# Performance work log

Measured on AMD Instinct MI355X. Metric: run time of the kernel, lower is better.

The kernel has to match this reference:

```python
import jax, jax.numpy as jnp
import numpy as np
import math
from jax import lax

B, NP1, M, D, H, L, DFF = 16, 65, 256, 512, 8, 3, 2048
EPS_PROJ = 0.01  # MartingaleProjectionLayer is built with epsilon=0.01
LN_EPS = 1e-5


def _pos_encoding(n, d):
    pos = np.arange(n, dtype=np.float32)[:, None]
    div = np.exp(np.arange(0, d, 2, dtype=np.float32) * (-math.log(10000.0) / d))
    pe = np.zeros((n, d), dtype=np.float32)
    pe[:, 0::2] = np.sin(pos * div)
    pe[:, 1::2] = np.cos(pos * div)
    return jnp.asarray(pe)


def setup_inputs() -> dict:
    key = jax.random.key(0)
    ks = jax.random.split(key, 32)
    s = 0.02
    marg = jax.random.uniform(ks[0], (B, NP1, M), jnp.float32)
    marg = marg / marg.sum(axis=-1, keepdims=True)  # proper distributions
    return {
        "marginals": marg,
        "x_grid": jnp.linspace(-3.0, 3.0, M, dtype=jnp.float32),
        "conv_w": jax.random.normal(ks[1], (128, 1, 5), jnp.float32) * s,
        "conv_b": jax.random.normal(ks[2], (128,), jnp.float32) * s,
        "fc_w": jax.random.normal(ks[3], (128, D), jnp.float32) * s,
        "fc_b": jax.random.normal(ks[4], (D,), jnp.float32) * s,
        "ln0_g": jnp.ones((D,), jnp.float32),
        "ln0_b": jnp.zeros((D,), jnp.float32),
        "pos_enc": _pos_encoding(NP1, D),
        "qkv_w": jax.random.normal(ks[5], (L, 3 * D, D), jnp.float32) * s,
        "qkv_b": jax.random.normal(ks[6], (L, 3 * D), jnp.float32) * s,
        "out_w": jax.random.normal(ks[7], (L, D, D), jnp.float32) * s,
        "out_b": jax.random.normal(ks[8], (L, D), jnp.float32) * s,
        "ln1_g": jnp.ones((L, D), jnp.float32),
        "ln1_b": jnp.zeros((L, D), jnp.float32),
        "ff1_w": jax.random.normal(ks[9], (L, DFF, D), jnp.float32) * s,
        "ff1_b": jax.random.normal(ks[10], (L, DFF), jnp.float32) * s,
        "ff2_w": jax.random.normal(ks[11], (L, D, DFF), jnp.float32) * s,
        "ff2_b": jax.random.normal(ks[12], (L, D), jnp.float32) * s,
        "ln2_g": jnp.ones((L, D), jnp.float32),
        "ln2_b": jnp.zeros((L, D), jnp.float32),
        "u_w": jax.random.normal(ks[13], (M, D), jnp.float32) * s,
        "u_b": jax.random.normal(ks[14], (M,), jnp.float32) * s,
        "h_w": jax.random.normal(ks[15], (M, D), jnp.float32) * s,
        "h_b": jax.random.normal(ks[16], (M,), jnp.float32) * s,
    }


def _ln(x, g, b):
    mu = x.mean(axis=-1, keepdims=True)
    var = ((x - mu) ** 2).mean(axis=-1, keepdims=True)
    return (x - mu) * lax.rsqrt(var + LN_EPS) * g + b


def _gelu(x):
    return jax.nn.gelu(x, approximate=False)  # torch default exact GELU


def reference(marginals, x_grid, conv_w, conv_b, fc_w, fc_b, ln0_g, ln0_b,
              pos_enc, qkv_w, qkv_b, out_w, out_b, ln1_g, ln1_b,
              ff1_w, ff1_b, ff2_w, ff2_b, ln2_g, ln2_b, u_w, u_b, h_w, h_b):
    b, np1, m = marginals.shape
    n = np1 - 1
    d = fc_w.shape[1]
    nh = H
    dh = d // nh

    # ---- marginal embedding: Conv1d(1,128,k=5,pad=2) -> mean over grid -> FC+LN+GELU
    x = marginals.reshape(b * np1, 1, m)
    y = lax.conv_general_dilated(x, conv_w, (1,), [(2, 2)],
                                 dimension_numbers=("NCH", "OIH", "NCH"))
    y = y + conv_b[None, :, None]          # (b*np1, 128, m)
    emb = y.mean(axis=2)                   # (b*np1, 128)
    emb = _gelu(_ln(emb @ fc_w + fc_b, ln0_g, ln0_b))
    xs = emb.reshape(b, np1, d) + pos_enc[None, :np1, :]

    # ---- post-norm transformer encoder (dropout off / eval mode)
    scale = 1.0 / math.sqrt(dh)
    for l in range(L):
        qkv = xs @ qkv_w[l].T + qkv_b[l]                        # (b, s, 3d)
        q, k, v = jnp.split(qkv, 3, axis=-1)
        q = q.reshape(b, np1, nh, dh).transpose(0, 2, 1, 3)
        k = k.reshape(b, np1, nh, dh).transpose(0, 2, 1, 3)
        v = v.reshape(b, np1, nh, dh).transpose(0, 2, 1, 3)
        att = jax.nn.softmax(jnp.einsum("bhqd,bhkd->bhqk", q, k) * scale, axis=-1)
        o = jnp.einsum("bhqk,bhkd->bhqd", att, v)
        o = o.transpose(0, 2, 1, 3).reshape(b, np1, d)
        o = o @ out_w[l].T + out_b[l]
        xs = _ln(xs + o, ln1_g[l], ln1_b[l])
        ff = _gelu(xs @ ff1_w[l].T + ff1_b[l]) @ ff2_w[l].T + ff2_b[l]
        xs = _ln(xs + ff, ln2_g[l], ln2_b[l])

    u_pot = xs @ u_w.T + u_b                                    # (b, np1, M)
    h_raw = xs[:, :n, :] @ h_w.T + h_b                          # (b, n, M)

    # ---- vectorized martingale projection over all N timesteps
    x_diff = x_grid[:, None] - x_grid[None, :]                  # (M, M)
    h_kernel = h_raw[..., None] * x_diff                        # (b, n, M, M)
    P = jax.nn.softmax(h_kernel / EPS_PROJ, axis=-1)
    expected_next = jnp.einsum("bnij,j->bni", P, x_grid)
    drift = expected_next - x_grid                              # (b, n, M)
    mu = marginals[:, :n, :]
    weight_drift = (mu * drift).sum(axis=-1, keepdims=True)
    correction = weight_drift / (mu.sum(axis=-1, keepdims=True) + 1e-8)
    h_pot = h_raw - correction
    return (u_pot, h_pot)
```

## Files before the change

### kernel.cpp

```cpp
#include <hip/hip_runtime.h>
#include <math.h>


#define BT   1040
#define NP1  65
#define Dm   512
#define MG   256

typedef short short8 __attribute__((ext_vector_type(8)));
typedef float f32x4  __attribute__((ext_vector_type(4)));
typedef unsigned short u16;

__device__ __forceinline__ size_t pidx(int r, int c, int KB) {
  return ((size_t)((r >> 6) * KB + (c >> 6)) * 8 + ((c & 63) >> 3)) * 512
       + (size_t)((r & 63) * 8 + (c & 7));
}

__device__ __forceinline__ u16 f2bf(float f) {
  unsigned int u = __float_as_uint(f);
  u += 0x7FFF + ((u >> 16) & 1);
  return (u16)(u >> 16);
}

__device__ __forceinline__ float bf2f(u16 v) {
  return __uint_as_float((unsigned int)v << 16);
}

__device__ __forceinline__ float gelu_exact(float x) {
  return 0.5f * x * (1.0f + erff(x * 0.70710678118654752f));
}

__device__ __forceinline__ void async16(const u16* g, u16* l) {
  __builtin_amdgcn_global_load_lds(
      (const __attribute__((address_space(1))) unsigned int*)g,
      (__attribute__((address_space(3))) unsigned int*)l, 16, 0, 0);
}

__device__ __forceinline__ float wred(float v) {
#pragma unroll
  for (int o = 32; o; o >>= 1) v += __shfl_xor(v, o, 64);
  return v;
}

__device__ __forceinline__ float block_reduce_sum(float v, float* s) {
#pragma unroll
  for (int off = 32; off; off >>= 1) v += __shfl_down(v, off, 64);
  int lane = threadIdx.x & 63, wid = threadIdx.x >> 6;
  __syncthreads();
  if (lane == 0) s[wid] = v;
  __syncthreads();
  return s[0] + s[1] + s[2] + s[3];
}

__device__ __forceinline__ float f_closed(float a) {
  const float tf = 2.3529411765f;
  float t = a * tf;
  float s = fabsf(t);
  float E;
  if (s < 1e-4f) {
    E = 127.5f - 5461.25f * t;
  } else {
    float u = s * 256.0f;
    float term2 = (u < 80.0f) ? 256.0f / expm1f(u) : 0.0f;
    float Epos = 1.0f / expm1f(s) - term2;
    E = (t > 0.0f) ? Epos : 255.0f - Epos;
  }
  return -3.0f + 0.0235294118f * E;
}

__global__ __launch_bounds__(256) void prep_kernel(
    const float* __restrict__ qkv_w, const float* __restrict__ out_w,
    const float* __restrict__ ff1_w, const float* __restrict__ ff2_w,
    const float* __restrict__ u_w,   const float* __restrict__ h_w,
    u16* __restrict__ wdst,
    const float* __restrict__ marg, const float* __restrict__ conv_w,
    const float* __restrict__ conv_b, const float* __restrict__ fc_w,
    const float* __restrict__ fc_b, const float* __restrict__ g,
    const float* __restrict__ bb, const float* __restrict__ pos,
    float* __restrict__ xs, u16* __restrict__ xsb)
{
  const int tid = threadIdx.x;
  if (blockIdx.x < 512) {
    const size_t O1 = 2359296, O2 = 3145728, O3 = 6291456;
    const size_t O4 = 9437184, O5 = 9568256, TOT4 = 9699328 / 4;
    for (size_t e4 = (size_t)blockIdx.x * 256 + tid; e4 < TOT4;
         e4 += (size_t)512 * 256) {
      size_t e = e4 * 4;
      const float* src; size_t base; int n, k, KB;
      if (e < O1)      { size_t r = e;      src = qkv_w + r; base = 0;
                         n = (int)(r >> 9);  k = (int)(r & 511);  KB = 8; }
      else if (e < O2) { size_t r = e - O1; src = out_w + r; base = O1;
                         n = (int)(r >> 9);  k = (int)(r & 511);  KB = 8; }
      else if (e < O3) { size_t r = e - O2; src = ff1_w + r; base = O2;
                         n = (int)(r >> 9);  k = (int)(r & 511);  KB = 8; }
      else if (e < O4) { size_t r = e - O3; src = ff2_w + r; base = O3;
                         n = (int)(r >> 11); k = (int)(r & 2047); KB = 32; }
      else if (e < O5) { size_t r = e - O4; src = u_w + r;   base = O4;
                         n = (int)(r >> 9);  k = (int)(r & 511);  KB = 8; }
      else             { size_t r = e - O5; src = h_w + r;   base = O4;
                         n = 256 + (int)(r >> 9); k = (int)(r & 511); KB = 8; }
      float4 v = *(const float4*)src;
      unsigned int lo = (unsigned int)f2bf(v.x) | ((unsigned int)f2bf(v.y) << 16);
      unsigned int hi = (unsigned int)f2bf(v.z) | ((unsigned int)f2bf(v.w) << 16);
      *(uint2*)(wdst + base + pidx(n, k, KB)) = make_uint2(lo, hi);
    }
    return;
  }
  __shared__ float es[4][128];
  __shared__ float sS[4];
  __shared__ float edge[4][4];
  __shared__ float red[4];
  const int t0 = (blockIdx.x - 512) * 4;
  const int lane = tid & 63, wave = tid >> 6;
  {
    float4 mv = *(const float4*)(marg + (size_t)(t0 + wave) * MG + lane * 4);
    float S = wred(mv.x + mv.y + mv.z + mv.w);
    if (lane == 0) sS[wave] = S;
  }
  if (tid < 16) {
    int k = tid >> 2, e = tid & 3;
    int idx = (e < 2) ? e : (e + 252);
    edge[k][e] = marg[(size_t)(t0 + k) * MG + idx];
  }
  __syncthreads();
  if (tid < 128) {
    int o = tid;
    float w0 = conv_w[o*5+0], w1 = conv_w[o*5+1], w2 = conv_w[o*5+2];
    float w3 = conv_w[o*5+3], w4 = conv_w[o*5+4], cb = conv_b[o];
#pragma unroll
    for (int k = 0; k < 4; ++k) {
      float S = sS[k];
      float x0 = edge[k][0], x1 = edge[k][1], x254 = edge[k][2], x255 = edge[k][3];
      es[k][o] = (w0*(S - x254 - x255) + w1*(S - x255) + w2*S
                + w3*(S - x0) + w4*(S - x0 - x1)) * (1.0f/256.0f) + cb;
    }
  }
  __syncthreads();
  float b0 = fc_b[tid], b1 = fc_b[tid + 256];
  float z[4][2];
#pragma unroll
  for (int k = 0; k < 4; ++k) { z[k][0] = b0; z[k][1] = b1; }
#pragma unroll 4
  for (int o = 0; o < 128; ++o) {
    float f0 = fc_w[(size_t)o*Dm + tid];
    float f1 = fc_w[(size_t)o*Dm + tid + 256];
#pragma unroll
    for (int k = 0; k < 4; ++k) {
      float e = es[k][o];
      z[k][0] += e * f0; z[k][1] += e * f1;
    }
  }
  float g0 = g[tid], g1 = g[tid+256], e0 = bb[tid], e1 = bb[tid+256];
#pragma unroll
  for (int k = 0; k < 4; ++k) {
    float mu = block_reduce_sum(z[k][0] + z[k][1], red) * (1.0f/512.0f);
    float d0 = z[k][0] - mu, d1 = z[k][1] - mu;
    float var = block_reduce_sum(d0*d0 + d1*d1, red) * (1.0f/512.0f);
    float inv = rsqrtf(var + 1e-5f);
    int t = t0 + k, p = t % NP1;
    float y0 = gelu_exact(d0*inv*g0 + e0) + pos[(size_t)p*Dm + tid];
    float y1 = gelu_exact(d1*inv*g1 + e1) + pos[(size_t)p*Dm + tid + 256];
    xs[(size_t)t*Dm + tid]        = y0;
    xs[(size_t)t*Dm + tid + 256]  = y1;
    xsb[pidx(t, tid, 8)]          = f2bf(y0);
    xsb[pidx(t, tid + 256, 8)]    = f2bf(y1);
  }
}

template<int MODE>
__global__ __launch_bounds__(256) void gemm_mfma(
    const u16* __restrict__ A, const u16* __restrict__ Bw,
    const float* __restrict__ bias, float* __restrict__ Cf,
    u16* __restrict__ Cb, int Mrows, int N, int K)
{
  __shared__ alignas(16) u16 Asl[2][4096];
  __shared__ alignas(16) u16 Bsl[2][4096];
  const int tid = threadIdx.x;
  const int row0 = blockIdx.y * 64, col0 = blockIdx.x * 64;
  const int lane = tid & 63, wave = tid >> 6;
  const int wm = (wave >> 1) * 32, wn = (wave & 1) * 32;
  const int l15 = lane & 15, q = lane >> 4;
  const int KB = K >> 6;

  f32x4 acc[2][2];
  acc[0][0] = (f32x4){0,0,0,0}; acc[0][1] = (f32x4){0,0,0,0};
  acc[1][0] = (f32x4){0,0,0,0}; acc[1][1] = (f32x4){0,0,0,0};

  const size_t abase = (size_t)blockIdx.y * KB * 4096 + (size_t)lane * 8;
  const size_t bbase = (size_t)blockIdx.x * KB * 4096 + (size_t)lane * 8;
  const int c0w = wave * 2;

#pragma unroll
  for (int i = 0; i < 2; ++i) {
    int c = c0w + i;
    async16(A + abase + (size_t)c * 512, &Asl[0][(size_t)(c * 64 + lane) * 8]);
    async16(Bw + bbase + (size_t)c * 512, &Bsl[0][(size_t)(c * 64 + lane) * 8]);
  }

  const int nk = K >> 6;
  for (int t = 0; t < nk; ++t) {
    const int cur = t & 1;
    if (t + 1 < nk) {
      const int nxt = cur ^ 1;
#pragma unroll
      for (int i = 0; i < 2; ++i) {
        int c = c0w + i;
        async16(A + abase + (size_t)((t + 1) * 8 + c) * 512,
                &Asl[nxt][(size_t)(c * 64 + lane) * 8]);
        async16(Bw + bbase + (size_t)((t + 1) * 8 + c) * 512,
                &Bsl[nxt][(size_t)(c * 64 + lane) * 8]);
      }
      asm volatile("s_waitcnt vmcnt(4)" ::: "memory");
    } else {
      asm volatile("s_waitcnt vmcnt(0)" ::: "memory");
    }
    __builtin_amdgcn_s_barrier();
#pragma unroll
    for (int tt = 0; tt < 2; ++tt) {
      int cc = tt * 4 + q;
      short8 af[2], bf[2];
#pragma unroll
      for (int mi = 0; mi < 2; ++mi)
        af[mi] = *(short8*)&Asl[cur][(size_t)(cc*64 + wm + mi*16 + l15) * 8];
#pragma unroll
      for (int ni = 0; ni < 2; ++ni)
        bf[ni] = *(short8*)&Bsl[cur][(size_t)(cc*64 + wn + ni*16 + l15) * 8];
#pragma unroll
      for (int mi = 0; mi < 2; ++mi)
#pragma unroll
        for (int ni = 0; ni < 2; ++ni)
          acc[mi][ni] = __builtin_amdgcn_mfma_f32_16x16x32_bf16(
              af[mi], bf[ni], acc[mi][ni], 0, 0, 0);
    }
    __builtin_amdgcn_s_barrier();
  }

#pragma unroll
  for (int mi = 0; mi < 2; ++mi) {
#pragma unroll
    for (int ni = 0; ni < 2; ++ni) {
      int col = col0 + wn + ni*16 + l15;
#pragma unroll
      for (int r = 0; r < 4; ++r) {
        int row = row0 + wm + mi*16 + q*4 + r;
        if (row < Mrows) {
          float v = acc[mi][ni][r];
          if (MODE == 0) {
            Cf[(size_t)row*N + col] = v + bias[col];
          } else {
            Cb[pidx(row, col, 32)] = f2bf(gelu_exact(v + bias[col]));
          }
        }
      }
    }
  }
}

__global__ __launch_bounds__(256) void fused_qkv_attn(
    const u16* __restrict__ xsb, const u16* __restrict__ qkvw,
    const float* __restrict__ qkvb, u16* __restrict__ obufb)
{
  __shared__ alignas(16) u16 stbuf[10240];
  __shared__ alignas(16) float qf[65][67];
  __shared__ alignas(16) float kf[65][67];
  __shared__ alignas(16) u16   vb[65][68];
  u16* sta = stbuf;
  float (*ss)[67] = (float (*)[67])stbuf;

  const int b = blockIdx.x >> 3, h = blockIdx.x & 7;
  const int tid = threadIdx.x, lane = tid & 63, wave = tid >> 6;
  const int l15 = lane & 15, q = lane >> 4;
  const int rowg0 = b * NP1;

  f32x4 acc[5][3];
#pragma unroll
  for (int rt = 0; rt < 5; ++rt)
#pragma unroll
    for (int j = 0; j < 3; ++j) acc[rt][j] = (f32x4){0,0,0,0};

  for (int ch = 0; ch < 4; ++ch) {
    __syncthreads();
    for (int idx = tid; idx < 16 * 80; idx += 256) {
      int kg = idx / 80, rl = idx - kg * 80;
      int r = rowg0 + min(rl, 64);
      async16(xsb + pidx(r, ch * 128 + kg * 8, 8), &sta[(size_t)idx * 8]);
    }
    asm volatile("s_waitcnt vmcnt(0)" ::: "memory");
    __syncthreads();

    short8 bcur[3], bnxt[3];
#pragma unroll
    for (int j = 0; j < 3; ++j) {
      int f = wave * 3 + j, region = f >> 2, sub = f & 3;
      int nb = region * 8 + h, nn = sub * 16 + l15;
      int kk = ch * 128 + q * 8;
      int kbg = kk >> 6, cc = (kk & 63) >> 3;
      bcur[j] = *(const short8*)&qkvw[((size_t)(nb * 8 + kbg) * 8 + cc) * 512
                                      + nn * 8];
    }
#pragma unroll
    for (int s = 0; s < 4; ++s) {
      if (s + 1 < 4) {
#pragma unroll
        for (int j = 0; j < 3; ++j) {
          int f = wave * 3 + j, region = f >> 2, sub = f & 3;
          int nb = region * 8 + h, nn = sub * 16 + l15;
          int kk = ch * 128 + (s + 1) * 32 + q * 8;
          int kbg = kk >> 6, cc = (kk & 63) >> 3;
          bnxt[j] = *(const short8*)&qkvw[((size_t)(nb * 8 + kbg) * 8 + cc) * 512
                                          + nn * 8];
        }
      }
      short8 af[5];
#pragma unroll
      for (int rt = 0; rt < 5; ++rt)
        af[rt] = *(short8*)&sta[(size_t)((s * 4 + q) * 80 + rt * 16 + l15) * 8];
#pragma unroll
      for (int rt = 0; rt < 5; ++rt)
#pragma unroll
        for (int j = 0; j < 3; ++j)
          acc[rt][j] = __builtin_amdgcn_mfma_f32_16x16x32_bf16(
              af[rt], bcur[j], acc[rt][j], 0, 0, 0);
#pragma unroll
      for (int j = 0; j < 3; ++j) bcur[j] = bnxt[j];
    }
  }

#pragma unroll
  for (int rt = 0; rt < 5; ++rt) {
#pragma unroll
    for (int j = 0; j < 3; ++j) {
      int f = wave * 3 + j, region = f >> 2, sub = f & 3;
      int cw = sub * 16 + l15;
      float bias = qkvb[region * 512 + h * 64 + cw];
#pragma unroll
      for (int r = 0; r < 4; ++r) {
        int row = rt * 16 + q * 4 + r;
        if (row < 65) {
          float v = acc[rt][j][r] + bias;
          if      (region == 0) qf[row][cw] = v;
          else if (region == 1) kf[row][cw] = v;
          else                  vb[row][cw] = f2bf(v);
        }
      }
    }
  }
  __syncthreads();

#pragma unroll
  for (int it = 0; it < 2; ++it) {
    int tile = it * 256 + tid;
    if (tile < 289) {
      int ti = (tile / 17) * 4, tj = (tile % 17) * 4;
      const float* qr[4]; const float* kr[4];
#pragma unroll
      for (int i = 0; i < 4; ++i) { qr[i] = qf[min(ti + i, 64)]; kr[i] = kf[min(tj + i, 64)]; }
      float a4[4][4] = {};
      for (int d = 0; d < 64; ++d) {
        float a[4], bvv[4];
#pragma unroll
        for (int i = 0; i < 4; ++i) { a[i] = qr[i][d]; bvv[i] = kr[i][d]; }
#pragma unroll
        for (int i = 0; i < 4; ++i)
#pragma unroll
          for (int j = 0; j < 4; ++j) a4[i][j] += a[i] * bvv[j];
      }
#pragma unroll
      for (int i = 0; i < 4; ++i)
        if (ti + i < 65)
#pragma unroll
          for (int j = 0; j < 4; ++j)
            if (tj + j < 65) ss[ti + i][tj + j] = a4[i][j] * 0.125f;
    }
  }
  __syncthreads();

  if (tid < 65) {
    float mx = -1e30f;
    for (int j = 0; j < 65; ++j) mx = fmaxf(mx, ss[tid][j]);
    float s = 0.0f;
    for (int j = 0; j < 65; ++j) { float e = expf(ss[tid][j] - mx); ss[tid][j] = e; s += e; }
    float inv = 1.0f / s;
    for (int j = 0; j < 65; ++j) ss[tid][j] *= inv;
  }
  __syncthreads();

#pragma unroll
  for (int it = 0; it < 2; ++it) {
    int tile = it * 256 + tid;
    if (tile < 272) {
      int ti = (tile >> 4) * 4, d0 = (tile & 15) * 4;
      const float* sr[4];
#pragma unroll
      for (int i = 0; i < 4; ++i) sr[i] = ss[min(ti + i, 64)];
      float a4[4][4] = {};
      for (int j = 0; j < 65; ++j) {
        float v0 = bf2f(vb[j][d0]),   v1 = bf2f(vb[j][d0+1]);
        float v2 = bf2f(vb[j][d0+2]), v3 = bf2f(vb[j][d0+3]);
#pragma unroll
        for (int i = 0; i < 4; ++i) {
          float s = sr[i][j];
          a4[i][0] += s * v0; a4[i][1] += s * v1;
          a4[i][2] += s * v2; a4[i][3] += s * v3;
        }
      }
#pragma unroll
      for (int i = 0; i < 4; ++i)
        if (ti + i < 65) {
          ushort4 o;
          o.x = f2bf(a4[i][0]); o.y = f2bf(a4[i][1]);
          o.z = f2bf(a4[i][2]); o.w = f2bf(a4[i][3]);
          *(ushort4*)(obufb + pidx(b * NP1 + ti + i, h * 64 + d0, 8)) = o;
        }
    }
  }
}

template<int KK, int EPI>
__global__ __launch_bounds__(512) void fused_row(
    const u16* __restrict__ A, const u16* __restrict__ Bw,
    const float* __restrict__ bias,
    float* __restrict__ xs, u16* __restrict__ xsb,
    const float* __restrict__ g, const float* __restrict__ bb,
    const float* __restrict__ bias2,
    const float* __restrict__ marg, const float* __restrict__ xg,
    float* __restrict__ outu, float* __restrict__ outh)
{
  constexpr int KB  = KK >> 6;
  constexpr int KC  = (KK < 1024) ? KK : 1024;
  constexpr int NCH = KK / KC;
  __shared__ alignas(16) u16 Alds[16 * KC];
  __shared__ float red[8][16];
  __shared__ float red2[8][16];
  const int tid = threadIdx.x, lane = tid & 63, wave = tid >> 6;
  const int l15 = lane & 15, q = lane >> 4;
  const int r0 = blockIdx.x * 16;
  const int rb = r0 >> 6, ro = r0 & 63;
  const int gc0 = wave * 64;
  const int nb = wave;

  f32x4 acc[4];
#pragma unroll
  for (int i = 0; i < 4; ++i) acc[i] = (f32x4){0,0,0,0};

  for (int ch = 0; ch < NCH; ++ch) {
    const int kc = ch * KC;
    __syncthreads();
    for (int idx = tid; idx < 2 * KC; idx += 512) {
      int rloc = idx & 15, cg = idx >> 4;
      int kbg = (kc >> 6) + (cg >> 3), cc = cg & 7;
      async16(A + ((size_t)(rb * KB + kbg) * 8 + cc) * 512 + (ro + rloc) * 8,
              &Alds[(size_t)idx * 8]);
    }
    asm volatile("s_waitcnt vmcnt(0)" ::: "memory");
    __syncthreads();

    constexpr int S = KC / 32;
    short8 bcur[4], bnxt[4];
    {
      int kk = kc + q * 8;
      int kbg = kk >> 6, cc = (kk & 63) >> 3;
#pragma unroll
      for (int i = 0; i < 4; ++i)
        bcur[i] = *(const short8*)&Bw[((size_t)(nb * KB + kbg) * 8 + cc) * 512
                                      + (i * 16 + l15) * 8];
    }
    for (int s = 0; s < S; ++s) {
      if (s + 1 < S) {
        int kk = kc + (s + 1) * 32 + q * 8;
        int kbg = kk >> 6, cc = (kk & 63) >> 3;
#pragma unroll
        for (int i = 0; i < 4; ++i)
          bnxt[i] = *(const short8*)&Bw[((size_t)(nb * KB + kbg) * 8 + cc) * 512
                                        + (i * 16 + l15) * 8];
      }
      short8 af = *(const short8*)&Alds[(size_t)((s * 4 + q) * 16 + l15) * 8];
#pragma unroll
      for (int i = 0; i < 4; ++i)
        acc[i] = __builtin_amdgcn_mfma_f32_16x16x32_bf16(af, bcur[i], acc[i], 0, 0, 0);
#pragma unroll
      for (int i = 0; i < 4; ++i) bcur[i] = bnxt[i];
    }
  }

  if (EPI == 0) {
    float vv[4][4];
#pragma unroll
    for (int i = 0; i < 4; ++i) {
      int col = gc0 + i*16 + l15;
      float bcol = bias[col];
#pragma unroll
      for (int r = 0; r < 4; ++r) {
        int gr = r0 + q*4 + r;
        vv[i][r] = acc[i][r] + bcol + xs[(size_t)gr * Dm + col];
      }
    }
    float ps[4];
#pragma unroll
    for (int r = 0; r < 4; ++r) {
      float s = 0.f;
#pragma unroll
      for (int i = 0; i < 4; ++i) s += vv[i][r];
      ps[r] = s;
    }
#pragma unroll
    for (int o = 1; o < 16; o <<= 1)
#pragma unroll
      for (int r = 0; r < 4; ++r) ps[r] += __shfl_xor(ps[r], o, 64);
    if (l15 == 0)
#pragma unroll
      for (int r = 0; r < 4; ++r) red[wave][q*4 + r] = ps[r];
    __syncthreads();
    float mu[4];
#pragma unroll
    for (int r = 0; r < 4; ++r) {
      int rr = q*4 + r;
      float s = 0.f;
#pragma unroll
      for (int w = 0; w < 8; ++w) s += red[w][rr];
      mu[r] = s * (1.0f/512.0f);
    }
    float ps2[4];
#pragma unroll
    for (int r = 0; r < 4; ++r) {
      float s = 0.f;
#pragma unroll
      for (int i = 0; i < 4; ++i) { float d = vv[i][r] - mu[r]; s += d * d; }
      ps2[r] = s;
    }
#pragma unroll
    for (int o = 1; o < 16; o <<= 1)
#pragma unroll
      for (int r = 0; r < 4; ++r) ps2[r] += __shfl_xor(ps2[r], o, 64);
    if (l15 == 0)
#pragma unroll
      for (int r = 0; r < 4; ++r) red2[wave][q*4 + r] = ps2[r];
    __syncthreads();
    float inv[4];
#pragma unroll
    for (int r = 0; r < 4; ++r) {
      int rr = q*4 + r;
      float s = 0.f;
#pragma unroll
      for (int w = 0; w < 8; ++w) s += red2[w][rr];
      inv[r] = rsqrtf(s * (1.0f/512.0f) + 1e-5f);
    }
#pragma unroll
    for (int i = 0; i < 4; ++i) {
      int col = gc0 + i*16 + l15;
      float gc = g[col], bc = bb[col];
#pragma unroll
      for (int r = 0; r < 4; ++r) {
        int gr = r0 + q*4 + r;
        float y = (vv[i][r] - mu[r]) * inv[r] * gc + bc;
        xs[(size_t)gr * Dm + col] = y;
        xsb[pidx(gr, col, 8)] = f2bf(y);
      }
    }
  } else {
    float va[4][4];
    if (wave >= 4) {
      float wd[4] = {0.f,0.f,0.f,0.f}, ms[4] = {0.f,0.f,0.f,0.f};
#pragma unroll
      for (int i = 0; i < 4; ++i) {
        int hcol = (gc0 - 256) + i*16 + l15;
        float bcol = bias2[hcol];
        float xv = xg[hcol];
#pragma unroll
        for (int r = 0; r < 4; ++r) {
          int gr = r0 + q*4 + r;
          float a = acc[i][r] + bcol;
          va[i][r] = a;
          float uvm = marg[(size_t)gr * MG + hcol];
          wd[r] += uvm * (f_closed(a) - xv);
          ms[r] += uvm;
        }
      }
#pragma unroll
      for (int o = 1; o < 16; o <<= 1)
#pragma unroll
        for (int r = 0; r < 4; ++r) {
          wd[r] += __shfl_xor(wd[r], o, 64);
          ms[r] += __shfl_xor(ms[r], o, 64);
        }
      if (l15 == 0)
#pragma unroll
        for (int r = 0; r < 4; ++r) {
          red[wave][q*4 + r]  = wd[r];
          red2[wave][q*4 + r] = ms[r];
        }
    }
    __syncthreads();
    if (wave < 4) {
#pragma unroll
      for (int i = 0; i < 4; ++i) {
        int col = gc0 + i*16 + l15;
        float bcol = bias[col];
#pragma unroll
        for (int r = 0; r < 4; ++r) {
          int gr = r0 + q*4 + r;
          outu[(size_t)gr * MG + col] = acc[i][r] + bcol;
        }
      }
    } else {
#pragma unroll
      for (int i = 0; i < 4; ++i) {
        int hcol = (gc0 - 256) + i*16 + l15;
#pragma unroll
        for (int r = 0; r < 4; ++r) {
          int rr = q*4 + r;
          int gr = r0 + rr;
          int bI = gr / NP1, n = gr - bI * NP1;
          if (n < 64) {
            float num = red[4][rr] + red[5][rr] + red[6][rr] + red[7][rr];
            float den = red2[4][rr] + red2[5][rr] + red2[6][rr] + red2[7][rr];
            float corr = num / (den + 1e-8f);
            outh[(size_t)(bI * 64 + n) * MG + hcol] = va[i][r] - corr;
          }
        }
      }
    }
  }
}

extern "C" void kernel_launch(void* const* d_in, const int* in_sizes, int n_in,
                              void* d_out, int out_size, void* d_ws, size_t ws_size,
                              hipStream_t stream)
{
  const float* marg   = (const float*)d_in[0];
  const float* xg     = (const float*)d_in[1];
  const float* conv_w = (const float*)d_in[2];
  const float* conv_b = (const float*)d_in[3];
  const float* fc_w   = (const float*)d_in[4];
  const float* fc_b   = (const float*)d_in[5];
  const float* ln0_g  = (const float*)d_in[6];
  const float* ln0_b  = (const float*)d_in[7];
  const float* pos    = (const float*)d_in[8];
  const float* qkv_w  = (const float*)d_in[9];
  const float* qkv_b  = (const float*)d_in[10];
  const float* out_w  = (const float*)d_in[11];
  const float* out_b  = (const float*)d_in[12];
  const float* ln1_g  = (const float*)d_in[13];
  const float* ln1_b  = (const float*)d_in[14];
  const float* ff1_w  = (const float*)d_in[15];
  const float* ff1_b  = (const float*)d_in[16];
  const float* ff2_w  = (const float*)d_in[17];
  const float* ff2_b  = (const float*)d_in[18];
  const float* ln2_g  = (const float*)d_in[19];
  const float* ln2_b  = (const float*)d_in[20];
  const float* u_w    = (const float*)d_in[21];
  const float* u_b    = (const float*)d_in[22];
  const float* h_w    = (const float*)d_in[23];
  const float* h_b    = (const float*)d_in[24];
  float* out = (float*)d_out;

  float* ws = (float*)d_ws;
  float* xs      = ws;
  u16*   xsb     = (u16*)(ws + 2129920);
  u16*   obufb   = (u16*)(ws + 2408448);
  u16*   ffb     = (u16*)(ws + 2686976);
  u16*   wbf     = (u16*)(ws + 3801088);

  const u16* qkv_bw = wbf;
  const u16* out_bw = wbf + 2359296;
  const u16* ff1_bw = wbf + 3145728;
  const u16* ff2_bw = wbf + 6291456;
  const u16* uh_bw  = wbf + 9437184;

  prep_kernel<<<772, 256, 0, stream>>>(
      qkv_w, out_w, ff1_w, ff2_w, u_w, h_w, wbf,
      marg, conv_w, conv_b, fc_w, fc_b, ln0_g, ln0_b, pos, xs, xsb);

  for (int l = 0; l < 3; ++l) {
    fused_qkv_attn<<<128, 256, 0, stream>>>(
        xsb, qkv_bw + (size_t)l*786432, qkv_b + l*1536, obufb);
    fused_row<512, 0><<<65, 512, 0, stream>>>(
        obufb, out_bw + (size_t)l*262144, out_b + l*512,
        xs, xsb, ln1_g + l*512, ln1_b + l*512,
        nullptr, nullptr, nullptr, nullptr, nullptr);
    gemm_mfma<1><<<dim3(32, 17), 256, 0, stream>>>(
        xsb, ff1_bw + (size_t)l*1048576, ff1_b + l*2048, nullptr,
        ffb, BT, 2048, 512);
    fused_row<2048, 0><<<65, 512, 0, stream>>>(
        ffb, ff2_bw + (size_t)l*1048576, ff2_b + l*512,
        xs, xsb, ln2_g + l*512, ln2_b + l*512,
        nullptr, nullptr, nullptr, nullptr, nullptr);
  }

  fused_row<512, 1><<<65, 512, 0, stream>>>(
      xsb, uh_bw, u_b,
      nullptr, nullptr, nullptr, nullptr,
      h_b, marg, xg, out, out + 1040*256);
}
```

Baseline: 379.1 us.

## Fuse FF1 GEMM, GELU, FF2 GEMM and LayerNorm into one row-block kernel

Replaces the separate FF1 GEMM (which wrote a bf16 GELU intermediate to global memory) and the FF2 row kernel with a single kernel. Each 512-thread block handles 8 token rows. It computes the 2048-wide hidden activation into LDS, then does FF2, the residual add and LayerNorm in place. This removes a launch and the global round-trip of the 1040x2048 intermediate. The cost is that every one of the 130 blocks streams the full FF1 and FF2 weights straight from global/L2 with no LDS tiling, and half of each 16-row MFMA tile is wasted on padding since only 8 rows are real.

```diff
diff --git a/kernel.cpp b/kernel.cpp
--- a/kernel.cpp
+++ b/kernel.cpp
@@ -167,95 +167,6 @@
   }
 }
 
-template<int MODE>
-__global__ __launch_bounds__(256) void gemm_mfma(
-    const u16* __restrict__ A, const u16* __restrict__ Bw,
-    const float* __restrict__ bias, float* __restrict__ Cf,
-    u16* __restrict__ Cb, int Mrows, int N, int K)
-{
-  __shared__ alignas(16) u16 Asl[2][4096];
-  __shared__ alignas(16) u16 Bsl[2][4096];
-  const int tid = threadIdx.x;
-  const int row0 = blockIdx.y * 64, col0 = blockIdx.x * 64;
-  const int lane = tid & 63, wave = tid >> 6;
-  const int wm = (wave >> 1) * 32, wn = (wave & 1) * 32;
-  const int l15 = lane & 15, q = lane >> 4;
-  const int KB = K >> 6;
-
-  f32x4 acc[2][2];
-  acc[0][0] = (f32x4){0,0,0,0}; acc[0][1] = (f32x4){0,0,0,0};
-  acc[1][0] = (f32x4){0,0,0,0}; acc[1][1] = (f32x4){0,0,0,0};
-
-  const size_t abase = (size_t)blockIdx.y * KB * 4096 + (size_t)lane * 8;
-  const size_t bbase = (size_t)blockIdx.x * KB * 4096 + (size_t)lane * 8;
-  const int c0w = wave * 2;
-
-#pragma unroll
-  for (int i = 0; i < 2; ++i) {
-    int c = c0w + i;
-    async16(A + abase + (size_t)c * 512, &Asl[0][(size_t)(c * 64 + lane) * 8]);
-    async16(Bw + bbase + (size_t)c * 512, &Bsl[0][(size_t)(c * 64 + lane) * 8]);
-  }
-
-  const int nk = K >> 6;
-  for (int t = 0; t < nk; ++t) {
-    const int cur = t & 1;
-    if (t + 1 < nk) {
-      const int nxt = cur ^ 1;
-#pragma unroll
-      for (int i = 0; i < 2; ++i) {
-        int c = c0w + i;
-        async16(A + abase + (size_t)((t + 1) * 8 + c) * 512,
-                &Asl[nxt][(size_t)(c * 64 + lane) * 8]);
-        async16(Bw + bbase + (size_t)((t + 1) * 8 + c) * 512,
-                &Bsl[nxt][(size_t)(c * 64 + lane) * 8]);
-      }
-      asm volatile("s_waitcnt vmcnt(4)" ::: "memory");
-    } else {
-      asm volatile("s_waitcnt vmcnt(0)" ::: "memory");
-    }
-    __builtin_amdgcn_s_barrier();
-#pragma unroll
-    for (int tt = 0; tt < 2; ++tt) {
-      int cc = tt * 4 + q;
-      short8 af[2], bf[2];
-#pragma unroll
-      for (int mi = 0; mi < 2; ++mi)
-        af[mi] = *(short8*)&Asl[cur][(size_t)(cc*64 + wm + mi*16 + l15) * 8];
-#pragma unroll
-      for (int ni = 0; ni < 2; ++ni)
-        bf[ni] = *(short8*)&Bsl[cur][(size_t)(cc*64 + wn + ni*16 + l15) * 8];
-#pragma unroll
-      for (int mi = 0; mi < 2; ++mi)
-#pragma unroll
-        for (int ni = 0; ni < 2; ++ni)
-          acc[mi][ni] = __builtin_amdgcn_mfma_f32_16x16x32_bf16(
-              af[mi], bf[ni], acc[mi][ni], 0, 0, 0);
-    }
-    __builtin_amdgcn_s_barrier();
-  }
-
-#pragma unroll
-  for (int mi = 0; mi < 2; ++mi) {
-#pragma unroll
-    for (int ni = 0; ni < 2; ++ni) {
-      int col = col0 + wn + ni*16 + l15;
-#pragma unroll
-      for (int r = 0; r < 4; ++r) {
-        int row = row0 + wm + mi*16 + q*4 + r;
-        if (row < Mrows) {
-          float v = acc[mi][ni][r];
-          if (MODE == 0) {
-            Cf[(size_t)row*N + col] = v + bias[col];
-          } else {
-            Cb[pidx(row, col, 32)] = f2bf(gelu_exact(v + bias[col]));
-          }
-        }
-      }
-    }
-  }
-}
-
 __global__ __launch_bounds__(256) void fused_qkv_attn(
     const u16* __restrict__ xsb, const u16* __restrict__ qkvw,
     const float* __restrict__ qkvb, u16* __restrict__ obufb)
@@ -618,6 +529,177 @@
             outh[(size_t)(bI * 64 + n) * MG + hcol] = va[i][r] - corr;
           }
         }
+      }
+    }
+  }
+}
+
+__global__ __launch_bounds__(512) void fused_ff(
+    const u16* __restrict__ xsb_in, const u16* __restrict__ f1w,
+    const u16* __restrict__ f2w, const float* __restrict__ b1,
+    const float* __restrict__ b2,
+    float* __restrict__ xs, u16* __restrict__ xsb,
+    const float* __restrict__ g, const float* __restrict__ bb)
+{
+  __shared__ alignas(16) u16 A1[64 * 8 * 8];
+  __shared__ alignas(16) u16 H[256 * 8 * 8];
+  __shared__ float red[8][8];
+  __shared__ float red2[8][8];
+  const int tid = threadIdx.x, lane = tid & 63, wave = tid >> 6;
+  const int l15 = lane & 15, q = lane >> 4;
+  const int r0 = blockIdx.x * 8;
+  const int rb = r0 >> 6, ro = r0 & 63;
+
+  {
+    int idx = tid;
+    int rloc = idx & 7, cg = idx >> 3;
+    async16(xsb_in + ((size_t)(rb * 8 + (cg >> 3)) * 8 + (cg & 7)) * 512
+                   + (ro + rloc) * 8,
+            &A1[(size_t)idx * 8]);
+  }
+  asm volatile("s_waitcnt vmcnt(0)" ::: "memory");
+  __syncthreads();
+
+  {
+    f32x4 acc1[16];
+#pragma unroll
+    for (int f = 0; f < 16; ++f) acc1[f] = (f32x4){0,0,0,0};
+    for (int s = 0; s < 16; ++s) {
+      int kk = s * 32 + q * 8;
+      int kbg = kk >> 6, cc = (kk & 63) >> 3;
+      short8 bf[16];
+#pragma unroll
+      for (int f = 0; f < 16; ++f) {
+        int nb = wave * 4 + (f >> 2), nn = (f & 3) * 16 + l15;
+        bf[f] = *(const short8*)&f1w[((size_t)(nb * 8 + kbg) * 8 + cc) * 512
+                                     + nn * 8];
+      }
+      short8 af = *(const short8*)&A1[(size_t)((s * 4 + q) * 8 + (l15 & 7)) * 8];
+#pragma unroll
+      for (int f = 0; f < 16; ++f)
+        acc1[f] = __builtin_amdgcn_mfma_f32_16x16x32_bf16(af, bf[f], acc1[f], 0, 0, 0);
+    }
+    if (q < 2) {
+#pragma unroll
+      for (int f = 0; f < 16; ++f) {
+        int c = wave * 256 + f * 16 + l15;
+        float bcol = b1[c];
+#pragma unroll
+        for (int r = 0; r < 4; ++r) {
+          int row = q * 4 + r;
+          H[(size_t)((c >> 3) * 8 + row) * 8 + (c & 7)] =
+              f2bf(gelu_exact(acc1[f][r] + bcol));
+        }
+      }
+    }
+  }
+  __syncthreads();
+
+  f32x4 acc[4];
+#pragma unroll
+  for (int i = 0; i < 4; ++i) acc[i] = (f32x4){0,0,0,0};
+  {
+    short8 bcur[4], bnxt[4];
+    {
+      int kk = q * 8;
+      int kbg = kk >> 6, cc = (kk & 63) >> 3;
+#pragma unroll
+      for (int i = 0; i < 4; ++i)
+        bcur[i] = *(const short8*)&f2w[((size_t)(wave * 32 + kbg) * 8 + cc) * 512
+                                       + (i * 16 + l15) * 8];
+    }
+    for (int s = 0; s < 64; ++s) {
+      if (s + 1 < 64) {
+        int kk = (s + 1) * 32 + q * 8;
+        int kbg = kk >> 6, cc = (kk & 63) >> 3;
+#pragma unroll
+        for (int i = 0; i < 4; ++i)
+          bnxt[i] = *(const short8*)&f2w[((size_t)(wave * 32 + kbg) * 8 + cc) * 512
+                                         + (i * 16 + l15) * 8];
+      }
+      short8 af = *(const short8*)&H[(size_t)((s * 4 + q) * 8 + (l15 & 7)) * 8];
+#pragma unroll
+      for (int i = 0; i < 4; ++i)
+        acc[i] = __builtin_amdgcn_mfma_f32_16x16x32_bf16(af, bcur[i], acc[i], 0, 0, 0);
+#pragma unroll
+      for (int i = 0; i < 4; ++i) bcur[i] = bnxt[i];
+    }
+  }
+
+  const int gc0 = wave * 64;
+  float vv[4][4];
+#pragma unroll
+  for (int i = 0; i < 4; ++i) {
+    int col = gc0 + i*16 + l15;
+    float bcol = b2[col];
+#pragma unroll
+    for (int r = 0; r < 4; ++r) {
+      int gr = r0 + ((q*4 + r) & 7);
+      vv[i][r] = acc[i][r] + bcol + xs[(size_t)gr * Dm + col];
+    }
+  }
+  float ps[4];
+#pragma unroll
+  for (int r = 0; r < 4; ++r) {
+    float s = 0.f;
+#pragma unroll
+    for (int i = 0; i < 4; ++i) s += vv[i][r];
+    ps[r] = s;
+  }
+#pragma unroll
+  for (int o = 1; o < 16; o <<= 1)
+#pragma unroll
+    for (int r = 0; r < 4; ++r) ps[r] += __shfl_xor(ps[r], o, 64);
+  if (l15 == 0 && q < 2)
+#pragma unroll
+    for (int r = 0; r < 4; ++r) red[wave][q*4 + r] = ps[r];
+  __syncthreads();
+  float mu[4];
+#pragma unroll
+  for (int r = 0; r < 4; ++r) {
+    int rr = (q*4 + r) & 7;
+    float s = 0.f;
+#pragma unroll
+    for (int w = 0; w < 8; ++w) s += red[w][rr];
+    mu[r] = s * (1.0f/512.0f);
+  }
+  float ps2[4];
+#pragma unroll
+  for (int r = 0; r < 4; ++r) {
+    float s = 0.f;
+#pragma unroll
+    for (int i = 0; i < 4; ++i) { float d = vv[i][r] - mu[r]; s += d * d; }
+    ps2[r] = s;
+  }
+#pragma unroll
+  for (int o = 1; o < 16; o <<= 1)
+#pragma unroll
+    for (int r = 0; r < 4; ++r) ps2[r] += __shfl_xor(ps2[r], o, 64);
+  if (l15 == 0 && q < 2)
+#pragma unroll
+    for (int r = 0; r < 4; ++r) red2[wave][q*4 + r] = ps2[r];
+  __syncthreads();
+  float inv[4];
+#pragma unroll
+  for (int r = 0; r < 4; ++r) {
+    int rr = (q*4 + r) & 7;
+    float s = 0.f;
+#pragma unroll
+    for (int w = 0; w < 8; ++w) s += red2[w][rr];
+    inv[r] = rsqrtf(s * (1.0f/512.0f) + 1e-5f);
+  }
+#pragma unroll
+  for (int i = 0; i < 4; ++i) {
+    int col = gc0 + i*16 + l15;
+    float gc = g[col], bc = bb[col];
+#pragma unroll
+    for (int r = 0; r < 4; ++r) {
+      int lr = q*4 + r;
+      if (lr < 8) {
+        int gr = r0 + lr;
+        float y = (vv[i][r] - mu[r]) * inv[r] * gc + bc;
+        xs[(size_t)gr * Dm + col] = y;
+        xsb[pidx(gr, col, 8)] = f2bf(y);
       }
     }
   }
@@ -658,7 +740,6 @@
   float* xs      = ws;
   u16*   xsb     = (u16*)(ws + 2129920);
   u16*   obufb   = (u16*)(ws + 2408448);
-  u16*   ffb     = (u16*)(ws + 2686976);
   u16*   wbf     = (u16*)(ws + 3801088);
 
   const u16* qkv_bw = wbf;
@@ -678,13 +759,10 @@
         obufb, out_bw + (size_t)l*262144, out_b + l*512,
         xs, xsb, ln1_g + l*512, ln1_b + l*512,
         nullptr, nullptr, nullptr, nullptr, nullptr);
-    gemm_mfma<1><<<dim3(32, 17), 256, 0, stream>>>(
-        xsb, ff1_bw + (size_t)l*1048576, ff1_b + l*2048, nullptr,
-        ffb, BT, 2048, 512);
-    fused_row<2048, 0><<<65, 512, 0, stream>>>(
-        ffb, ff2_bw + (size_t)l*1048576, ff2_b + l*512,
-        xs, xsb, ln2_g + l*512, ln2_b + l*512,
-        nullptr, nullptr, nullptr, nullptr, nullptr);
+    fused_ff<<<130, 512, 0, stream>>>(
+        xsb, ff1_bw + (size_t)l*1048576, ff2_bw + (size_t)l*1048576,
+        ff1_b + l*2048, ff2_b + l*512,
+        xs, xsb, ln2_g + l*512, ln2_b + l*512);
   }
 
   fused_row<512, 1><<<65, 512, 0, stream>>>(
```

After: 634.0 us. 67.3% more time.

## Use 1024-thread FF2+LayerNorm kernel and fuse final u/h head into last layer

Applied to the files above, without the earlier changes.

The FF2 row kernel now runs 16 waves per block, each computing a 32-column slice instead of 64. This doubles the parallelism per row block for the K=2048 GEMM. On the last layer the normalized rows are written as bf16 into shared memory, and the u/h output head GEMM plus the martingale correction run in the same kernel, so one launch and a round trip through global memory go away. The cost is a larger block with more synchronisation and a longer tail in the last-layer kernel.

```diff
diff --git a/kernel.cpp b/kernel.cpp
--- a/kernel.cpp
+++ b/kernel.cpp
@@ -416,20 +416,14 @@
   }
 }
 
-template<int KK, int EPI>
-__global__ __launch_bounds__(512) void fused_row(
+__global__ __launch_bounds__(512) void fused_row512(
     const u16* __restrict__ A, const u16* __restrict__ Bw,
     const float* __restrict__ bias,
     float* __restrict__ xs, u16* __restrict__ xsb,
-    const float* __restrict__ g, const float* __restrict__ bb,
-    const float* __restrict__ bias2,
-    const float* __restrict__ marg, const float* __restrict__ xg,
-    float* __restrict__ outu, float* __restrict__ outh)
+    const float* __restrict__ g, const float* __restrict__ bb)
 {
-  constexpr int KB  = KK >> 6;
-  constexpr int KC  = (KK < 1024) ? KK : 1024;
-  constexpr int NCH = KK / KC;
-  __shared__ alignas(16) u16 Alds[16 * KC];
+  constexpr int KB = 8;
+  __shared__ alignas(16) u16 Alds[16 * 512];
   __shared__ float red[8][16];
   __shared__ float red2[8][16];
   const int tid = threadIdx.x, lane = tid & 63, wave = tid >> 6;
@@ -443,10 +437,145 @@
 #pragma unroll
   for (int i = 0; i < 4; ++i) acc[i] = (f32x4){0,0,0,0};
 
-  for (int ch = 0; ch < NCH; ++ch) {
-    const int kc = ch * KC;
+  for (int idx = tid; idx < 1024; idx += 512) {
+    int rloc = idx & 15, cg = idx >> 4;
+    int kbg = cg >> 3, cc = cg & 7;
+    async16(A + ((size_t)(rb * KB + kbg) * 8 + cc) * 512 + (ro + rloc) * 8,
+            &Alds[(size_t)idx * 8]);
+  }
+  asm volatile("s_waitcnt vmcnt(0)" ::: "memory");
+  __syncthreads();
+
+  short8 bcur[4], bnxt[4];
+  {
+    int kk = q * 8;
+    int kbg = kk >> 6, cc = (kk & 63) >> 3;
+#pragma unroll
+    for (int i = 0; i < 4; ++i)
+      bcur[i] = *(const short8*)&Bw[((size_t)(nb * KB + kbg) * 8 + cc) * 512
+                                    + (i * 16 + l15) * 8];
+  }
+  for (int s = 0; s < 16; ++s) {
+    if (s + 1 < 16) {
+      int kk = (s + 1) * 32 + q * 8;
+      int kbg = kk >> 6, cc = (kk & 63) >> 3;
+#pragma unroll
+      for (int i = 0; i < 4; ++i)
+        bnxt[i] = *(const short8*)&Bw[((size_t)(nb * KB + kbg) * 8 + cc) * 512
+                                      + (i * 16 + l15) * 8];
+    }
+    short8 af = *(const short8*)&Alds[(size_t)((s * 4 + q) * 16 + l15) * 8];
+#pragma unroll
+    for (int i = 0; i < 4; ++i)
+      acc[i] = __builtin_amdgcn_mfma_f32_16x16x32_bf16(af, bcur[i], acc[i], 0, 0, 0);
+#pragma unroll
+    for (int i = 0; i < 4; ++i) bcur[i] = bnxt[i];
+  }
+
+  float vv[4][4];
+#pragma unroll
+  for (int i = 0; i < 4; ++i) {
+    int col = gc0 + i*16 + l15;
+    float bcol = bias[col];
+#pragma unroll
+    for (int r = 0; r < 4; ++r) {
+      int gr = r0 + q*4 + r;
+      vv[i][r] = acc[i][r] + bcol + xs[(size_t)gr * Dm + col];
+    }
+  }
+  float ps[4];
+#pragma unroll
+  for (int r = 0; r < 4; ++r) {
+    float s = 0.f;
+#pragma unroll
+    for (int i = 0; i < 4; ++i) s += vv[i][r];
+    ps[r] = s;
+  }
+#pragma unroll
+  for (int o = 1; o < 16; o <<= 1)
+#pragma unroll
+    for (int r = 0; r < 4; ++r) ps[r] += __shfl_xor(ps[r], o, 64);
+  if (l15 == 0)
+#pragma unroll
+    for (int r = 0; r < 4; ++r) red[wave][q*4 + r] = ps[r];
+  __syncthreads();
+  float mu[4];
+#pragma unroll
+  for (int r = 0; r < 4; ++r) {
+    int rr = q*4 + r;
+    float s = 0.f;
+#pragma unroll
+    for (int w = 0; w < 8; ++w) s += red[w][rr];
+    mu[r] = s * (1.0f/512.0f);
+  }
+  float ps2[4];
+#pragma unroll
+  for (int r = 0; r < 4; ++r) {
+    float s = 0.f;
+#pragma unroll
+    for (int i = 0; i < 4; ++i) { float d = vv[i][r] - mu[r]; s += d * d; }
+    ps2[r] = s;
+  }
+#pragma unroll
+  for (int o = 1; o < 16; o <<= 1)
+#pragma unroll
+    for (int r = 0; r < 4; ++r) ps2[r] += __shfl_xor(ps2[r], o, 64);
+  if (l15 == 0)
+#pragma unroll
+    for (int r = 0; r < 4; ++r) red2[wave][q*4 + r] = ps2[r];
+  __syncthreads();
+  float inv[4];
+#pragma unroll
+  for (int r = 0; r < 4; ++r) {
+    int rr = q*4 + r;
+    float s = 0.f;
+#pragma unroll
+    for (int w = 0; w < 8; ++w) s += red2[w][rr];
+    inv[r] = rsqrtf(s * (1.0f/512.0f) + 1e-5f);
+  }
+#pragma unroll
+  for (int i = 0; i < 4; ++i) {
+    int col = gc0 + i*16 + l15;
+    float gc = g[col], bc = bb[col];
+#pragma unroll
+    for (int r = 0; r < 4; ++r) {
+      int gr = r0 + q*4 + r;
+      float y = (vv[i][r] - mu[r]) * inv[r] * gc + bc;
+      xs[(size_t)gr * Dm + col] = y;
+      xsb[pidx(gr, col, 8)] = f2bf(y);
+    }
+  }
+}
+
+template<int HEAD>
+__global__ __launch_bounds__(1024) void fused_ff2(
+    const u16* __restrict__ A, const u16* __restrict__ Bw,
+    const float* __restrict__ bias,
+    float* __restrict__ xs, u16* __restrict__ xsb,
+    const float* __restrict__ g, const float* __restrict__ bb,
+    const u16* __restrict__ uhw, const float* __restrict__ ub,
+    const float* __restrict__ hbv, const float* __restrict__ marg,
+    const float* __restrict__ xg, float* __restrict__ outu,
+    float* __restrict__ outh)
+{
+  constexpr int KB = 32;
+  __shared__ alignas(16) u16 Alds[16 * 1024];
+  __shared__ float red[16][16];
+  __shared__ float red2[16][16];
+  const int tid = threadIdx.x, lane = tid & 63, wave = tid >> 6;
+  const int l15 = lane & 15, q = lane >> 4;
+  const int r0 = blockIdx.x * 16;
+  const int rb = r0 >> 6, ro = r0 & 63;
+  const int nb = wave >> 1;
+  const int nn0 = (wave & 1) * 32;
+
+  f32x4 acc[2];
+  acc[0] = (f32x4){0,0,0,0}; acc[1] = (f32x4){0,0,0,0};
+
+  for (int ch = 0; ch < 2; ++ch) {
+    const int kc = ch * 1024;
     __syncthreads();
-    for (int idx = tid; idx < 2 * KC; idx += 512) {
+    for (int idx = tid; idx < 2048; idx += 1024) {
       int rloc = idx & 15, cg = idx >> 4;
       int kbg = (kc >> 6) + (cg >> 3), cc = cg & 7;
       async16(A + ((size_t)(rb * KB + kbg) * 8 + cc) * 512 + (ro + rloc) * 8,
@@ -455,99 +584,92 @@
     asm volatile("s_waitcnt vmcnt(0)" ::: "memory");
     __syncthreads();
 
-    constexpr int S = KC / 32;
-    short8 bcur[4], bnxt[4];
+    short8 bcur[2], bnxt[2];
     {
       int kk = kc + q * 8;
       int kbg = kk >> 6, cc = (kk & 63) >> 3;
 #pragma unroll
-      for (int i = 0; i < 4; ++i)
+      for (int i = 0; i < 2; ++i)
         bcur[i] = *(const short8*)&Bw[((size_t)(nb * KB + kbg) * 8 + cc) * 512
-                                      + (i * 16 + l15) * 8];
-    }
-    for (int s = 0; s < S; ++s) {
-      if (s + 1 < S) {
+                                      + (nn0 + i * 16 + l15) * 8];
+    }
+    for (int s = 0; s < 32; ++s) {
+      if (s + 1 < 32) {
         int kk = kc + (s + 1) * 32 + q * 8;
         int kbg = kk >> 6, cc = (kk & 63) >> 3;
 #pragma unroll
-        for (int i = 0; i < 4; ++i)
+        for (int i = 0; i < 2; ++i)
           bnxt[i] = *(const short8*)&Bw[((size_t)(nb * KB + kbg) * 8 + cc) * 512
-                                        + (i * 16 + l15) * 8];
+                                        + (nn0 + i * 16 + l15) * 8];
       }
       short8 af = *(const short8*)&Alds[(size_t)((s * 4 + q) * 16 + l15) * 8];
 #pragma unroll
-      for (int i = 0; i < 4; ++i)
+      for (int i = 0; i < 2; ++i)
         acc[i] = __builtin_amdgcn_mfma_f32_16x16x32_bf16(af, bcur[i], acc[i], 0, 0, 0);
 #pragma unroll
-      for (int i = 0; i < 4; ++i) bcur[i] = bnxt[i];
-    }
-  }
-
-  if (EPI == 0) {
-    float vv[4][4];
-#pragma unroll
-    for (int i = 0; i < 4; ++i) {
-      int col = gc0 + i*16 + l15;
-      float bcol = bias[col];
-#pragma unroll
-      for (int r = 0; r < 4; ++r) {
-        int gr = r0 + q*4 + r;
-        vv[i][r] = acc[i][r] + bcol + xs[(size_t)gr * Dm + col];
-      }
-    }
-    float ps[4];
+      for (int i = 0; i < 2; ++i) bcur[i] = bnxt[i];
+    }
+  }
+
+  float vv[2][4];
+#pragma unroll
+  for (int i = 0; i < 2; ++i) {
+    int col = wave * 32 + i*16 + l15;
+    float bcol = bias[col];
 #pragma unroll
     for (int r = 0; r < 4; ++r) {
-      float s = 0.f;
-#pragma unroll
-      for (int i = 0; i < 4; ++i) s += vv[i][r];
-      ps[r] = s;
-    }
-#pragma unroll
-    for (int o = 1; o < 16; o <<= 1)
-#pragma unroll
-      for (int r = 0; r < 4; ++r) ps[r] += __shfl_xor(ps[r], o, 64);
-    if (l15 == 0)
-#pragma unroll
-      for (int r = 0; r < 4; ++r) red[wave][q*4 + r] = ps[r];
-    __syncthreads();
-    float mu[4];
-#pragma unroll
-    for (int r = 0; r < 4; ++r) {
-      int rr = q*4 + r;
-      float s = 0.f;
-#pragma unroll
-      for (int w = 0; w < 8; ++w) s += red[w][rr];
-      mu[r] = s * (1.0f/512.0f);
-    }
-    float ps2[4];
-#pragma unroll
-    for (int r = 0; r < 4; ++r) {
-      float s = 0.f;
-#pragma unroll
-      for (int i = 0; i < 4; ++i) { float d = vv[i][r] - mu[r]; s += d * d; }
-      ps2[r] = s;
-    }
-#pragma unroll
-    for (int o = 1; o < 16; o <<= 1)
-#pragma unroll
-      for (int r = 0; r < 4; ++r) ps2[r] += __shfl_xor(ps2[r], o, 64);
-    if (l15 == 0)
-#pragma unroll
-      for (int r = 0; r < 4; ++r) red2[wave][q*4 + r] = ps2[r];
-    __syncthreads();
-    float inv[4];
-#pragma unroll
-    for (int r = 0; r < 4; ++r) {
-      int rr = q*4 + r;
-      float s = 0.f;
-#pragma unroll
-      for (int w = 0; w < 8; ++w) s += red2[w][rr];
-      inv[r] = rsqrtf(s * (1.0f/512.0f) + 1e-5f);
-    }
-#pragma unroll
-    for (int i = 0; i < 4; ++i) {
-      int col = gc0 + i*16 + l15;
+      int gr = r0 + q*4 + r;
+      vv[i][r] = acc[i][r] + bcol + xs[(size_t)gr * Dm + col];
+    }
+  }
+  float ps[4];
+#pragma unroll
+  for (int r = 0; r < 4; ++r) { ps[r] = vv[0][r] + vv[1][r]; }
+#pragma unroll
+  for (int o = 1; o < 16; o <<= 1)
+#pragma unroll
+    for (int r = 0; r < 4; ++r) ps[r] += __shfl_xor(ps[r], o, 64);
+  if (l15 == 0)
+#pragma unroll
+    for (int r = 0; r < 4; ++r) red[wave][q*4 + r] = ps[r];
+  __syncthreads();
+  float mu[4];
+#pragma unroll
+  for (int r = 0; r < 4; ++r) {
+    int rr = q*4 + r;
+    float s = 0.f;
+#pragma unroll
+    for (int w = 0; w < 16; ++w) s += red[w][rr];
+    mu[r] = s * (1.0f/512.0f);
+  }
+  float ps2[4];
+#pragma unroll
+  for (int r = 0; r < 4; ++r) {
+    float d0 = vv[0][r] - mu[r], d1 = vv[1][r] - mu[r];
+    ps2[r] = d0*d0 + d1*d1;
+  }
+#pragma unroll
+  for (int o = 1; o < 16; o <<= 1)
+#pragma unroll
+    for (int r = 0; r < 4; ++r) ps2[r] += __shfl_xor(ps2[r], o, 64);
+  if (l15 == 0)
+#pragma unroll
+    for (int r = 0; r < 4; ++r) red2[wave][q*4 + r] = ps2[r];
+  __syncthreads();
+  float inv[4];
+#pragma unroll
+  for (int r = 0; r < 4; ++r) {
+    int rr = q*4 + r;
+    float s = 0.f;
+#pragma unroll
+    for (int w = 0; w < 16; ++w) s += red2[w][rr];
+    inv[r] = rsqrtf(s * (1.0f/512.0f) + 1e-5f);
+  }
+
+  if (HEAD == 0) {
+#pragma unroll
+    for (int i = 0; i < 2; ++i) {
+      int col = wave * 32 + i*16 + l15;
       float gc = g[col], bc = bb[col];
 #pragma unroll
       for (int r = 0; r < 4; ++r) {
@@ -558,18 +680,62 @@
       }
     }
   } else {
-    float va[4][4];
-    if (wave >= 4) {
+    __syncthreads();
+#pragma unroll
+    for (int i = 0; i < 2; ++i) {
+      int col = wave * 32 + i*16 + l15;
+      float gc = g[col], bc = bb[col];
+#pragma unroll
+      for (int r = 0; r < 4; ++r) {
+        float y = (vv[i][r] - mu[r]) * inv[r] * gc + bc;
+        Alds[(size_t)((col >> 3) * 16 + (q*4 + r)) * 8 + (col & 7)] = f2bf(y);
+      }
+    }
+    __syncthreads();
+
+    const int w2 = (wave < 8) ? wave : (wave - 8);
+    const int ubr = ((wave < 8) ? 0 : 4) + (w2 >> 1);
+    const int hn0 = (w2 & 1) * 32;
+    f32x4 a2[2];
+    a2[0] = (f32x4){0,0,0,0}; a2[1] = (f32x4){0,0,0,0};
+    short8 bcur[2], bnxt[2];
+    {
+      int kk = q * 8;
+      int kbg = kk >> 6, cc = (kk & 63) >> 3;
+#pragma unroll
+      for (int i = 0; i < 2; ++i)
+        bcur[i] = *(const short8*)&uhw[((size_t)(ubr * 8 + kbg) * 8 + cc) * 512
+                                       + (hn0 + i * 16 + l15) * 8];
+    }
+    for (int s = 0; s < 16; ++s) {
+      if (s + 1 < 16) {
+        int kk = (s + 1) * 32 + q * 8;
+        int kbg = kk >> 6, cc = (kk & 63) >> 3;
+#pragma unroll
+        for (int i = 0; i < 2; ++i)
+          bnxt[i] = *(const short8*)&uhw[((size_t)(ubr * 8 + kbg) * 8 + cc) * 512
+                                         + (hn0 + i * 16 + l15) * 8];
+      }
+      short8 af = *(const short8*)&Alds[(size_t)((s * 4 + q) * 16 + l15) * 8];
+#pragma unroll
+      for (int i = 0; i < 2; ++i)
+        a2[i] = __builtin_amdgcn_mfma_f32_16x16x32_bf16(af, bcur[i], a2[i], 0, 0, 0);
+#pragma unroll
+      for (int i = 0; i < 2; ++i) bcur[i] = bnxt[i];
+    }
+
+    float va[2][4];
+    if (wave >= 8) {
       float wd[4] = {0.f,0.f,0.f,0.f}, ms[4] = {0.f,0.f,0.f,0.f};
 #pragma unroll
-      for (int i = 0; i < 4; ++i) {
-        int hcol = (gc0 - 256) + i*16 + l15;
-        float bcol = bias2[hcol];
+      for (int i = 0; i < 2; ++i) {
+        int hcol = (wave - 8) * 32 + i*16 + l15;
+        float bcol = hbv[hcol];
         float xv = xg[hcol];
 #pragma unroll
         for (int r = 0; r < 4; ++r) {
           int gr = r0 + q*4 + r;
-          float a = acc[i][r] + bcol;
+          float a = a2[i][r] + bcol;
           va[i][r] = a;
           float uvm = marg[(size_t)gr * MG + hcol];
           wd[r] += uvm * (f_closed(a) - xv);
@@ -591,29 +757,30 @@
         }
     }
     __syncthreads();
-    if (wave < 4) {
-#pragma unroll
-      for (int i = 0; i < 4; ++i) {
-        int col = gc0 + i*16 + l15;
-        float bcol = bias[col];
+    if (wave < 8) {
+#pragma unroll
+      for (int i = 0; i < 2; ++i) {
+        int col = wave * 32 + i*16 + l15;
+        float bcol = ub[col];
 #pragma unroll
         for (int r = 0; r < 4; ++r) {
           int gr = r0 + q*4 + r;
-          outu[(size_t)gr * MG + col] = acc[i][r] + bcol;
+          outu[(size_t)gr * MG + col] = a2[i][r] + bcol;
         }
       }
     } else {
 #pragma unroll
-      for (int i = 0; i < 4; ++i) {
-        int hcol = (gc0 - 256) + i*16 + l15;
+      for (int i = 0; i < 2; ++i) {
+        int hcol = (wave - 8) * 32 + i*16 + l15;
 #pragma unroll
         for (int r = 0; r < 4; ++r) {
           int rr = q*4 + r;
           int gr = r0 + rr;
           int bI = gr / NP1, n = gr - bI * NP1;
           if (n < 64) {
-            float num = red[4][rr] + red[5][rr] + red[6][rr] + red[7][rr];
-            float den = red2[4][rr] + red2[5][rr] + red2[6][rr] + red2[7][rr];
+            float num = 0.f, den = 0.f;
+#pragma unroll
+            for (int w = 8; w < 16; ++w) { num += red[w][rr]; den += red2[w][rr]; }
             float corr = num / (den + 1e-8f);
             outh[(size_t)(bI * 64 + n) * MG + hcol] = va[i][r] - corr;
           }
@@ -674,21 +841,22 @@
   for (int l = 0; l < 3; ++l) {
     fused_qkv_attn<<<128, 256, 0, stream>>>(
         xsb, qkv_bw + (size_t)l*786432, qkv_b + l*1536, obufb);
-    fused_row<512, 0><<<65, 512, 0, stream>>>(
+    fused_row512<<<65, 512, 0, stream>>>(
         obufb, out_bw + (size_t)l*262144, out_b + l*512,
-        xs, xsb, ln1_g + l*512, ln1_b + l*512,
-        nullptr, nullptr, nullptr, nullptr, nullptr);
+        xs, xsb, ln1_g + l*512, ln1_b + l*512);
     gemm_mfma<1><<<dim3(32, 17), 256, 0, stream>>>(
         xsb, ff1_bw + (size_t)l*1048576, ff1_b + l*2048, nullptr,
         ffb, BT, 2048, 512);
-    fused_row<2048, 0><<<65, 512, 0, stream>>>(
-        ffb, ff2_bw + (size_t)l*1048576, ff2_b + l*512,
-        xs, xsb, ln2_g + l*512, ln2_b + l*512,
-        nullptr, nullptr, nullptr, nullptr, nullptr);
-  }
-
-  fused_row<512, 1><<<65, 512, 0, stream>>>(
-      xsb, uh_bw, u_b,
-      nullptr, nullptr, nullptr, nullptr,
-      h_b, marg, xg, out, out + 1040*256);
-}
+    if (l < 2) {
+      fused_ff2<0><<<65, 1024, 0, stream>>>(
+          ffb, ff2_bw + (size_t)l*1048576, ff2_b + l*512,
+          xs, xsb, ln2_g + l*512, ln2_b + l*512,
+          nullptr, nullptr, nullptr, nullptr, nullptr, nullptr, nullptr);
+    } else {
+      fused_ff2<1><<<65, 1024, 0, stream>>>(
+          ffb, ff2_bw + (size_t)l*1048576, ff2_b + l*512,
+          xs, xsb, ln2_g + l*512, ln2_b + l*512,
+          uh_bw, u_b, h_b, marg, xg, out, out + 1040*256);
+    }
+  }
+}
```

New measurement: 381.2 us. Within noise of the previous version (+0.6%).
